# Kernel tuning notes

Measured on AMD Instinct MI355X. Metric: run time of the kernel, lower is better.

## Reference

```python
import jax, jax.numpy as jnp
import numpy as np

N = 10000
E = 320000

def _glorot(key, fan_in, fan_out):
    s = jnp.sqrt(2.0 / (fan_in + fan_out)).astype(jnp.float32)
    return jax.random.normal(key, (fan_in, fan_out), dtype=jnp.float32) * s

def setup_inputs() -> dict:
    key = jax.random.key(0)
    ks = iter(jax.random.split(key, 40))
    inp = {}
    for i in range(3):
        inp[f"feature{i}"] = jax.random.normal(next(ks), (N, 512), dtype=jnp.float32)
    for name in ["g0", "g1", "g2", "g"]:
        inp[name + "_src"] = jax.random.randint(next(ks), (E,), 0, N, dtype=jnp.int32)
        inp[name + "_dst"] = jax.random.randint(next(ks), (E,), 0, N, dtype=jnp.int32)
    # per-view GCN stacks: in->512 (relu), 512->256 (identity)
    for v in range(3):
        inp[f"w{v}_0"] = _glorot(next(ks), 512, 512)
        inp[f"b{v}_0"] = jnp.zeros((512,), jnp.float32)
        inp[f"w{v}_1"] = _glorot(next(ks), 512, 256)
        inp[f"b{v}_1"] = jnp.zeros((256,), jnp.float32)
    # FeatureFusion: three 256x256 weights (torch.randn init) + Linear(256,256)
    for i in (1, 2, 3):
        inp[f"fw{i}"] = jax.random.normal(next(ks), (256, 256), dtype=jnp.float32)
    inp["fcw"] = _glorot(next(ks), 256, 256)
    inp["fcb"] = jnp.zeros((256,), jnp.float32)
    # fusion-graph GCN stack: 256->256 (relu), 256->128 (identity)
    inp["wm_0"] = _glorot(next(ks), 256, 256)
    inp["bm_0"] = jnp.zeros((256,), jnp.float32)
    inp["wm_1"] = _glorot(next(ks), 256, 128)
    inp["bm_1"] = jnp.zeros((128,), jnp.float32)
    # InnerProductDecoder weight (xavier uniform -> use glorot normal surrogate)
    inp["decw"] = _glorot(next(ks), 128, 128)
    return inp

def _gcn(src, dst, x, W, b, act):
    # DGL GraphConv norm='both': act(D_in^{-1/2} A D_out^{-1/2} x W + b)
    ones = jnp.ones(src.shape, jnp.float32)
    deg_out = jax.ops.segment_sum(ones, src, num_segments=N)
    deg_in = jax.ops.segment_sum(ones, dst, num_segments=N)
    n_out = jnp.where(deg_out > 0, jax.lax.rsqrt(jnp.maximum(deg_out, 1.0)), 0.0)
    n_in = jnp.where(deg_in > 0, jax.lax.rsqrt(jnp.maximum(deg_in, 1.0)), 0.0)
    h = (x @ W) * n_out[:, None]                        # [N, out] (mult W first: in>=out)
    agg = jax.ops.segment_sum(h[src], dst, num_segments=N)
    return act(agg * n_in[:, None] + b)

def reference(feature0, feature1, feature2,
              g0_src, g0_dst, g1_src, g1_dst, g2_src, g2_dst, g_src, g_dst,
              w0_0, b0_0, w0_1, b0_1, w1_0, b1_0, w1_1, b1_1, w2_0, b2_0, w2_1, b2_1,
              fw1, fw2, fw3, fcw, fcb, wm_0, bm_0, wm_1, bm_1, decw):
    relu = jax.nn.relu
    ident = lambda t: t
    h0 = _gcn(g0_src, g0_dst, _gcn(g0_src, g0_dst, feature0, w0_0, b0_0, relu), w0_1, b0_1, ident)
    h1 = _gcn(g1_src, g1_dst, _gcn(g1_src, g1_dst, feature1, w1_0, b1_0, relu), w1_1, b1_1, ident)
    h2 = _gcn(g2_src, g2_dst, _gcn(g2_src, g2_dst, feature2, w2_0, b2_0, relu), w2_1, b2_1, ident)
    # FeatureFusion
    y = h0 @ fw1 + h1 @ fw2 + h2 @ fw3
    xh = y @ fcw + fcb
    # fusion graph with self loops (dgl.add_self_loop)
    loop = jnp.arange(N, dtype=jnp.int32)
    gs = jnp.concatenate([g_src, loop])
    gd = jnp.concatenate([g_dst, loop])
    xh = _gcn(gs, gd, xh, wm_0, bm_0, relu)
    xh = _gcn(gs, gd, xh, wm_1, bm_1, ident)
    # InnerProductDecoder (identical for each of the 3 views)
    adj = jax.nn.sigmoid((xh @ decw) @ xh.T)            # [N, N]
    return adj, adj, adj, xh
```

## Files before the change

kernel.cpp:

```cpp
#include <hip/hip_runtime.h>
#include <hip/hip_bf16.h>
#include <cstdint>
#include <cstddef>

typedef __attribute__((ext_vector_type(8))) short s16x8;
typedef __attribute__((ext_vector_type(4))) float f32x4;


__device__ inline float sigmoidf_fast(float x) {
    return 1.0f / (1.0f + __expf(-x));
}

__device__ inline ushort f2bf_bits(float x) {
    __hip_bfloat16 h = __float2bfloat16(x);
    return *reinterpret_cast<ushort*>(&h);
}

__device__ inline uint pk2bf(float a, float b) {
    return (uint)f2bf_bits(a) | ((uint)f2bf_bits(b) << 16);
}


__global__ void f2bf3(const float* __restrict__ s0, const float* __restrict__ s1,
                      const float* __restrict__ s2, ushort* __restrict__ dst, int n4) {
    int z = blockIdx.y;
    const float* src = z == 0 ? s0 : (z == 1 ? s1 : s2);
    int i = blockIdx.x * 256 + threadIdx.x;
    if (i < n4) {
        float4 v = ((const float4*)src)[i];
        uint2 o;
        o.x = pk2bf(v.x, v.y);
        o.y = pk2bf(v.z, v.w);
        ((uint2*)(dst + (size_t)z * n4 * 4))[i] = o;
    }
}

__global__ void wtrans3(const float* __restrict__ s0, const float* __restrict__ s1,
                        const float* __restrict__ s2, ushort* __restrict__ dst,
                        int K, int NC, int ldDst, int colOffPerZ, size_t dstStrideZ) {
    int z = blockIdx.y;
    const float* src = z == 0 ? s0 : (z == 1 ? s1 : s2);
    int i = blockIdx.x * 256 + threadIdx.x;
    if (i >= K * NC) return;
    int k = i / NC, n = i - k * NC;
    dst[(size_t)z * dstStrideZ + (size_t)n * ldDst + colOffPerZ * z + k] = f2bf_bits(src[i]);
}


__global__ void count_all(const int* __restrict__ s0, const int* __restrict__ d0,
                          const int* __restrict__ s1, const int* __restrict__ d1,
                          const int* __restrict__ s2, const int* __restrict__ d2,
                          const int* __restrict__ s3, const int* __restrict__ d3,
                          int* __restrict__ cntOut, int* __restrict__ cntIn, int E, int N) {
    int i = blockIdx.x * 256 + threadIdx.x;
    if (i >= E) return;
    atomicAdd(&cntOut[s0[i]], 1);          atomicAdd(&cntIn[d0[i]], 1);
    atomicAdd(&cntOut[N + s1[i]], 1);      atomicAdd(&cntIn[N + d1[i]], 1);
    atomicAdd(&cntOut[2 * N + s2[i]], 1);  atomicAdd(&cntIn[2 * N + d2[i]], 1);
    atomicAdd(&cntOut[3 * N + s3[i]], 1);  atomicAdd(&cntIn[3 * N + d3[i]], 1);
}

__global__ void norm_all(const int* __restrict__ cntOut, const int* __restrict__ cntIn,
                         float* __restrict__ norms, int N) {
    int i = blockIdx.x * 256 + threadIdx.x;
    if (i >= 8 * N) return;
    int g = i / (2 * N);
    int rem = i - g * 2 * N;
    int half = rem / N;
    int r = rem - half * N;
    int c = (half ? cntIn : cntOut)[g * N + r] + (g == 3 ? 1 : 0);
    norms[i] = c > 0 ? rsqrtf((float)c) : 0.0f;
}


__global__ void scan4(const int* __restrict__ cntIn, int* __restrict__ rp4, int N) {
    __shared__ int partial[1024];
    int g = blockIdx.x;
    const int* counts = cntIn + (size_t)g * N;
    int* rowptr = rp4 + (size_t)g * (N + 1);
    int tid = threadIdx.x;
    int per = (N + 1023) >> 10;
    int start = tid * per;
    int s = 0;
    for (int i = 0; i < per; ++i) {
        int idx = start + i;
        if (idx < N) s += counts[idx];
    }
    partial[tid] = s;
    __syncthreads();
    for (int off = 1; off < 1024; off <<= 1) {
        int v = (tid >= off) ? partial[tid - off] : 0;
        __syncthreads();
        partial[tid] += v;
        __syncthreads();
    }
    int run = (tid > 0) ? partial[tid - 1] : 0;
    for (int i = 0; i < per; ++i) {
        int idx = start + i;
        if (idx < N) { rowptr[idx] = run; run += counts[idx]; }
    }
    if (tid == 1023) rowptr[N] = partial[1023];
}

__global__ void scatter4(const int* __restrict__ s0, const int* __restrict__ d0,
                         const int* __restrict__ s1, const int* __restrict__ d1,
                         const int* __restrict__ s2, const int* __restrict__ d2,
                         const int* __restrict__ s3, const int* __restrict__ d3,
                         const int* __restrict__ rp4, int* __restrict__ cursor4,
                         int* __restrict__ col4, int E, int N) {
    int g = blockIdx.y;
    const int* ss[4] = { s0, s1, s2, s3 };
    const int* dd[4] = { d0, d1, d2, d3 };
    int i = blockIdx.x * 256 + threadIdx.x;
    if (i >= E) return;
    int d = dd[g][i];
    int pos = atomicAdd(&cursor4[g * N + d], 1);
    col4[(size_t)g * E + rp4[(size_t)g * (N + 1) + d] + pos] = ss[g][i];
}


template<int HAS_SCALE, int HAS_BIAS>
__global__ __launch_bounds__(256) void gemm_bf16(
    const ushort* __restrict__ A, const ushort* __restrict__ BT,
    const float* __restrict__ rowscale, const float* __restrict__ bias,
    ushort* __restrict__ C, int M, int K, int NC,
    size_t aStride, size_t btStride, size_t cStride, int sStride)
{
    int v = blockIdx.z;
    A += (size_t)v * aStride;
    BT += (size_t)v * btStride;
    C += (size_t)v * cStride;
    if (HAS_SCALE) rowscale += (size_t)v * sStride;

    __shared__ ushort As[128 * 64];
    __shared__ ushort Bs[128 * 64];
    int tid = threadIdx.x;
    int wave = tid >> 6, lane = tid & 63;
    int wr = wave >> 1, wc = wave & 1;
    int rowBase = blockIdx.y * 128, colBase = blockIdx.x * 128;
    int lr = lane & 15, kg = lane >> 4;

    f32x4 acc[4][4] = {};

    for (int k0 = 0; k0 < K; k0 += 64) {
#pragma unroll
        for (int i = 0; i < 4; ++i) {
            int id = i * 256 + tid;
            int row = id >> 3;
            int co  = (id & 7) << 3;
            int boff = ((row * 64 + co) << 1) ^ ((row & 7) << 4);
            int ar = rowBase + row; if (ar >= M) ar = M - 1;
            uint4 av = *(const uint4*)(A + (size_t)ar * K + k0 + co);
            *(uint4*)((char*)As + boff) = av;
            int bc = colBase + row;
            uint4 bv = *(const uint4*)(BT + (size_t)bc * K + k0 + co);
            *(uint4*)((char*)Bs + boff) = bv;
        }
        __syncthreads();
#pragma unroll
        for (int ks = 0; ks < 2; ++ks) {
            s16x8 afr[4], bfr[4];
#pragma unroll
            for (int m = 0; m < 4; ++m) {
                int fr = wr * 64 + m * 16 + lr;
                int boff = ((fr * 64 + ks * 32 + kg * 8) << 1) ^ ((fr & 7) << 4);
                afr[m] = *(const s16x8*)((char*)As + boff);
            }
#pragma unroll
            for (int n = 0; n < 4; ++n) {
                int fc = wc * 64 + n * 16 + lr;
                int boff = ((fc * 64 + ks * 32 + kg * 8) << 1) ^ ((fc & 7) << 4);
                bfr[n] = *(const s16x8*)((char*)Bs + boff);
            }
#pragma unroll
            for (int m = 0; m < 4; ++m)
#pragma unroll
                for (int n = 0; n < 4; ++n)
                    acc[m][n] = __builtin_amdgcn_mfma_f32_16x16x32_bf16(afr[m], bfr[n], acc[m][n], 0, 0, 0);
        }
        __syncthreads();
    }

#pragma unroll
    for (int m = 0; m < 4; ++m) {
#pragma unroll
        for (int i = 0; i < 4; ++i) {
            int r = rowBase + wr * 64 + m * 16 + kg * 4 + i;
            if (r >= M) continue;
            float s = HAS_SCALE ? rowscale[r] : 1.0f;
#pragma unroll
            for (int n = 0; n < 4; ++n) {
                int c = colBase + wc * 64 + n * 16 + lr;
                float vv = acc[m][n][i] * s;
                if (HAS_BIAS) vv += bias[c];
                C[(size_t)r * NC + c] = f2bf_bits(vv);
            }
        }
    }
}


#define ACC8(u) { acc[0]+=__uint_as_float(u.x<<16); acc[1]+=__uint_as_float(u.x&0xffff0000u); \
                  acc[2]+=__uint_as_float(u.y<<16); acc[3]+=__uint_as_float(u.y&0xffff0000u); \
                  acc[4]+=__uint_as_float(u.z<<16); acc[5]+=__uint_as_float(u.z&0xffff0000u); \
                  acc[6]+=__uint_as_float(u.w<<16); acc[7]+=__uint_as_float(u.w&0xffff0000u); }

template<int W, int RELU, int SELF, int OUTF32>
__global__ __launch_bounds__(256) void spmm_bf16(
    const int* __restrict__ rp4, const int* __restrict__ col4,
    const ushort* __restrict__ hB, const float* __restrict__ normB,
    const float* __restrict__ b0v, const float* __restrict__ b1v, const float* __restrict__ b2v,
    ushort* __restrict__ outB, float* __restrict__ outf,
    int M, int E, size_t hStride, int ninStride, size_t outStride, int ldOut, int colOffPerV)
{
    constexpr int TPR = W / 8;
    constexpr int RPB = 256 / TPR;
    int v = blockIdx.y;
    const int* rowptr = rp4 + (size_t)v * (M + 1);
    const int* col = col4 + (size_t)v * E;
    const ushort* h = hB + (size_t)v * hStride;
    const float* n_in = normB + (size_t)v * ninStride + M;
    const float* bias = (v == 0) ? b0v : (v == 1 ? b1v : b2v);
    ushort* outb = outB + (size_t)v * outStride;
    int cOff = colOffPerV * v;

    int lpr = threadIdx.x & (TPR - 1);
    int r = blockIdx.x * RPB + (threadIdx.x / TPR);
    if (r >= M) return;
    int c = lpr * 8;

    float acc[8] = {};
    int beg = rowptr[r], end = rowptr[r + 1];
    int j = beg;
    for (; j + 3 < end; j += 4) {
        int sA = col[j], sB = col[j + 1], sC = col[j + 2], sD = col[j + 3];
        uint4 uA = *(const uint4*)(h + (size_t)sA * W + c);
        uint4 uB = *(const uint4*)(h + (size_t)sB * W + c);
        uint4 uC = *(const uint4*)(h + (size_t)sC * W + c);
        uint4 uD = *(const uint4*)(h + (size_t)sD * W + c);
        ACC8(uA); ACC8(uB); ACC8(uC); ACC8(uD);
    }
    for (; j < end; ++j) {
        int s = col[j];
        uint4 u = *(const uint4*)(h + (size_t)s * W + c);
        ACC8(u);
    }
    if (SELF) {
        uint4 u = *(const uint4*)(h + (size_t)r * W + c);
        ACC8(u);
    }
    float ni = n_in[r];
    float o[8];
    float4 bb0 = *(const float4*)(bias + c);
    float4 bb1 = *(const float4*)(bias + c + 4);
    o[0] = acc[0] * ni + bb0.x; o[1] = acc[1] * ni + bb0.y;
    o[2] = acc[2] * ni + bb0.z; o[3] = acc[3] * ni + bb0.w;
    o[4] = acc[4] * ni + bb1.x; o[5] = acc[5] * ni + bb1.y;
    o[6] = acc[6] * ni + bb1.z; o[7] = acc[7] * ni + bb1.w;
    if (RELU) {
#pragma unroll
        for (int q = 0; q < 8; ++q) o[q] = fmaxf(o[q], 0.f);
    }
    uint4 ob;
    ob.x = pk2bf(o[0], o[1]); ob.y = pk2bf(o[2], o[3]);
    ob.z = pk2bf(o[4], o[5]); ob.w = pk2bf(o[6], o[7]);
    *(uint4*)(outb + (size_t)r * ldOut + cOff + c) = ob;
    if (OUTF32) {
        *(float4*)(outf + (size_t)r * W + c) = make_float4(o[0], o[1], o[2], o[3]);
        *(float4*)(outf + (size_t)r * W + c + 4) = make_float4(o[4], o[5], o[6], o[7]);
    }
}


__global__ __launch_bounds__(256) void adj_mfma(
    const ushort* __restrict__ Zb, const ushort* __restrict__ Xb,
    float* __restrict__ out, int M)
{
    int wave = threadIdx.x >> 6;
    int lane = threadIdx.x & 63;
    int wr = wave >> 1, wc = wave & 1;
    int rowBase = blockIdx.y * 128 + wr * 64;
    int colBase = blockIdx.x * 128 + wc * 64;
    int lr = lane & 15;
    int kg = lane >> 4;

    f32x4 acc[4][4] = {};

    int ar[4], bc[4];
#pragma unroll
    for (int m = 0; m < 4; ++m) {
        int r = rowBase + m * 16 + lr; ar[m] = (r < M) ? r : (M - 1);
        int c = colBase + m * 16 + lr; bc[m] = (c < M) ? c : (M - 1);
    }

#pragma unroll
    for (int ks = 0; ks < 4; ++ks) {
        s16x8 afr[4], bfr[4];
#pragma unroll
        for (int m = 0; m < 4; ++m)
            afr[m] = *(const s16x8*)(Zb + (size_t)ar[m] * 128 + ks * 32 + kg * 8);
#pragma unroll
        for (int n = 0; n < 4; ++n)
            bfr[n] = *(const s16x8*)(Xb + (size_t)bc[n] * 128 + ks * 32 + kg * 8);
#pragma unroll
        for (int m = 0; m < 4; ++m)
#pragma unroll
            for (int n = 0; n < 4; ++n)
                acc[m][n] = __builtin_amdgcn_mfma_f32_16x16x32_bf16(afr[m], bfr[n], acc[m][n], 0, 0, 0);
    }

    size_t NN = (size_t)M * M;
#pragma unroll
    for (int m = 0; m < 4; ++m) {
#pragma unroll
        for (int i = 0; i < 4; ++i) {
            int r = rowBase + m * 16 + kg * 4 + i;
            if (r >= M) continue;
            float* rowp = out + (size_t)r * M;
#pragma unroll
            for (int n = 0; n < 4; ++n) {
                int c = colBase + n * 16 + lr;
                if (c >= M) continue;
                float v = sigmoidf_fast(acc[m][n][i]);
                __builtin_nontemporal_store(v, rowp + c);
                __builtin_nontemporal_store(v, rowp + c + NN);
                __builtin_nontemporal_store(v, rowp + c + 2 * NN);
            }
        }
    }
}


extern "C" void kernel_launch(void* const* d_in, const int* in_sizes, int n_in,
                              void* d_out, int out_size, void* d_ws, size_t ws_size,
                              hipStream_t stream)
{
    const int N = in_sizes[0] / 512;
    const int E = in_sizes[3];

    const float* feat[3] = { (const float*)d_in[0], (const float*)d_in[1], (const float*)d_in[2] };
    const int* gsrc[4] = { (const int*)d_in[3], (const int*)d_in[5], (const int*)d_in[7], (const int*)d_in[9] };
    const int* gdst[4] = { (const int*)d_in[4], (const int*)d_in[6], (const int*)d_in[8], (const int*)d_in[10] };
    const float* W0[3] = { (const float*)d_in[11], (const float*)d_in[15], (const float*)d_in[19] };
    const float* B0[3] = { (const float*)d_in[12], (const float*)d_in[16], (const float*)d_in[20] };
    const float* W1[3] = { (const float*)d_in[13], (const float*)d_in[17], (const float*)d_in[21] };
    const float* B1[3] = { (const float*)d_in[14], (const float*)d_in[18], (const float*)d_in[22] };
    const float* fw[3] = { (const float*)d_in[23], (const float*)d_in[24], (const float*)d_in[25] };
    const float* fcw = (const float*)d_in[26];
    const float* fcb = (const float*)d_in[27];
    const float* wm0 = (const float*)d_in[28];
    const float* bm0 = (const float*)d_in[29];
    const float* wm1 = (const float*)d_in[30];
    const float* bm1 = (const float*)d_in[31];
    const float* decw = (const float*)d_in[32];
    float* out = (float*)d_out;

    uint8_t* p = (uint8_t*)d_ws;
    auto alloc = [&](size_t bytes) { void* r = p; p += (bytes + 255) & ~(size_t)255; return r; };

    float*  norms   = (float*)alloc((size_t)8 * N * 4);
    ushort* featb   = (ushort*)alloc((size_t)3 * N * 512 * 2);
    ushort* w0T     = (ushort*)alloc((size_t)3 * 512 * 512 * 2);
    ushort* w1T     = (ushort*)alloc((size_t)3 * 256 * 512 * 2);
    ushort* fwT     = (ushort*)alloc((size_t)256 * 768 * 2);
    ushort* fcT     = (ushort*)alloc((size_t)256 * 256 * 2);
    ushort* wm0T    = (ushort*)alloc((size_t)256 * 256 * 2);
    ushort* wm1T    = (ushort*)alloc((size_t)128 * 256 * 2);
    ushort* decT    = (ushort*)alloc((size_t)128 * 128 * 2);
    ushort* h512_3  = (ushort*)alloc((size_t)3 * N * 512 * 2);
    ushort* hb512_3 = (ushort*)alloc((size_t)3 * N * 512 * 2);
    ushort* h256_3  = (ushort*)alloc((size_t)3 * N * 256 * 2);
    ushort* hvcat   = (ushort*)alloc((size_t)N * 768 * 2);
    ushort* ybuf    = (ushort*)alloc((size_t)N * 256 * 2);
    ushort* xh256   = (ushort*)alloc((size_t)N * 256 * 2);
    ushort* m256    = (ushort*)alloc((size_t)N * 256 * 2);
    ushort* xh1     = (ushort*)alloc((size_t)N * 256 * 2);
    ushort* h128    = (ushort*)alloc((size_t)N * 128 * 2);
    ushort* xb      = (ushort*)alloc((size_t)N * 128 * 2);
    ushort* zb      = (ushort*)alloc((size_t)N * 128 * 2);
    int* cntOut     = (int*)alloc((size_t)4 * N * 4);
    int* cntIn      = (int*)alloc((size_t)4 * N * 4);
    int* cursor4    = (int*)alloc((size_t)4 * N * 4);
    int* rp4        = (int*)alloc((size_t)4 * (N + 1) * 4);
    int* col4       = (int*)alloc((size_t)4 * E * 4);

    {
        dim3 g((N * 512 / 4 + 255) / 256, 3);
        f2bf3<<<g, 256, 0, stream>>>(feat[0], feat[1], feat[2], featb, N * 512 / 4);
    }
    wtrans3<<<dim3((512 * 512 + 255) / 256, 3), 256, 0, stream>>>(W0[0], W0[1], W0[2], w0T, 512, 512, 512, 0, (size_t)512 * 512);
    wtrans3<<<dim3((512 * 256 + 255) / 256, 3), 256, 0, stream>>>(W1[0], W1[1], W1[2], w1T, 512, 256, 512, 0, (size_t)256 * 512);
    wtrans3<<<dim3((256 * 256 + 255) / 256, 3), 256, 0, stream>>>(fw[0], fw[1], fw[2], fwT, 256, 256, 768, 256, 0);
    wtrans3<<<dim3((256 * 256 + 255) / 256, 1), 256, 0, stream>>>(fcw, fcw, fcw, fcT, 256, 256, 256, 0, 0);
    wtrans3<<<dim3((256 * 256 + 255) / 256, 1), 256, 0, stream>>>(wm0, wm0, wm0, wm0T, 256, 256, 256, 0, 0);
    wtrans3<<<dim3((256 * 128 + 255) / 256, 1), 256, 0, stream>>>(wm1, wm1, wm1, wm1T, 256, 128, 256, 0, 0);
    wtrans3<<<dim3((128 * 128 + 255) / 256, 1), 256, 0, stream>>>(decw, decw, decw, decT, 128, 128, 128, 0, 0);

    hipMemsetAsync(cntOut, 0, (size_t)12 * N * 4, stream);
    count_all<<<(E + 255) / 256, 256, 0, stream>>>(
        gsrc[0], gdst[0], gsrc[1], gdst[1], gsrc[2], gdst[2], gsrc[3], gdst[3], cntOut, cntIn, E, N);
    norm_all<<<(8 * N + 255) / 256, 256, 0, stream>>>(cntOut, cntIn, norms, N);
    scan4<<<4, 1024, 0, stream>>>(cntIn, rp4, N);
    scatter4<<<dim3((E + 255) / 256, 4), 256, 0, stream>>>(
        gsrc[0], gdst[0], gsrc[1], gdst[1], gsrc[2], gdst[2], gsrc[3], gdst[3],
        rp4, cursor4, col4, E, N);

    gemm_bf16<1, 0><<<dim3(4, (N + 127) / 128, 3), 256, 0, stream>>>(
        featb, w0T, norms, nullptr, h512_3, N, 512, 512,
        (size_t)N * 512, (size_t)512 * 512, (size_t)N * 512, 2 * N);
    spmm_bf16<512, 1, 0, 0><<<dim3((N + 3) / 4, 3), 256, 0, stream>>>(
        rp4, col4, h512_3, norms, B0[0], B0[1], B0[2], hb512_3, nullptr,
        N, E, (size_t)N * 512, 2 * N, (size_t)N * 512, 512, 0);
    gemm_bf16<1, 0><<<dim3(2, (N + 127) / 128, 3), 256, 0, stream>>>(
        hb512_3, w1T, norms, nullptr, h256_3, N, 512, 256,
        (size_t)N * 512, (size_t)256 * 512, (size_t)N * 256, 2 * N);
    spmm_bf16<256, 0, 0, 0><<<dim3((N + 7) / 8, 3), 256, 0, stream>>>(
        rp4, col4, h256_3, norms, B1[0], B1[1], B1[2], hvcat, nullptr,
        N, E, (size_t)N * 256, 2 * N, 0, 768, 256);

    gemm_bf16<0, 0><<<dim3(2, (N + 127) / 128, 1), 256, 0, stream>>>(
        hvcat, fwT, nullptr, nullptr, ybuf, N, 768, 256, 0, 0, 0, 0);
    gemm_bf16<0, 1><<<dim3(2, (N + 127) / 128, 1), 256, 0, stream>>>(
        ybuf, fcT, nullptr, fcb, xh256, N, 256, 256, 0, 0, 0, 0);

    const int* rpF = rp4 + 3 * (N + 1);
    const int* colF = col4 + (size_t)3 * E;
    gemm_bf16<1, 0><<<dim3(2, (N + 127) / 128, 1), 256, 0, stream>>>(
        xh256, wm0T, norms + 6 * N, nullptr, m256, N, 256, 256, 0, 0, 0, 0);
    spmm_bf16<256, 1, 1, 0><<<dim3((N + 7) / 8, 1), 256, 0, stream>>>(
        rpF, colF, m256, norms + 6 * N, bm0, bm0, bm0, xh1, nullptr,
        N, E, 0, 0, 0, 256, 0);
    gemm_bf16<1, 0><<<dim3(1, (N + 127) / 128, 1), 256, 0, stream>>>(
        xh1, wm1T, norms + 6 * N, nullptr, h128, N, 256, 128, 0, 0, 0, 0);
    float* xhf = out + (size_t)3 * N * N;
    spmm_bf16<128, 0, 1, 1><<<dim3((N + 15) / 16, 1), 256, 0, stream>>>(
        rpF, colF, h128, norms + 6 * N, bm1, bm1, bm1, xb, xhf,
        N, E, 0, 0, 0, 128, 0);

    gemm_bf16<0, 0><<<dim3(1, (N + 127) / 128, 1), 256, 0, stream>>>(
        xb, decT, nullptr, nullptr, zb, N, 128, 128, 0, 0, 0, 0);
    dim3 agrid((N + 127) / 128, (N + 127) / 128);
    adj_mfma<<<agrid, 256, 0, stream>>>(zb, xb, out, N);
}
```

Before: 904.2 us.

## Fold fusion weights into a single effective weight and merge prep kernels

Result: no change. 895.2 us (-1.0%).

```diff
diff --git a/kernel.cpp b/kernel.cpp
--- a/kernel.cpp
+++ b/kernel.cpp
@@ -18,6 +18,62 @@
 
 __device__ inline uint pk2bf(float a, float b) {
     return (uint)f2bf_bits(a) | ((uint)f2bf_bits(b) << 16);
+}
+
+
+struct PrepArgs {
+    int4* zeroPtr; int nZero4;
+    const float* tsrc[8]; ushort* tdst[8];
+    int tK[8], tNC[8], tld[8];
+    int tBase[9];
+    const float* fc; const float* wm0; const float* fcb;
+    float* T1;
+    int zBlocks, wBlocks, tBlocks;
+};
+
+__global__ __launch_bounds__(256) void prep_misc(PrepArgs a) {
+    int b = blockIdx.x;
+    int tid = threadIdx.x;
+    if (b < a.zBlocks) {
+        int i = b * 256 + tid;
+        if (i < a.nZero4) a.zeroPtr[i] = make_int4(0, 0, 0, 0);
+        return;
+    }
+    b -= a.zBlocks;
+    if (b < a.wBlocks) {
+        int j = 0;
+        while (!(b >= a.tBase[j] && b < a.tBase[j + 1])) ++j;
+        int e = (b - a.tBase[j]) * 256 + tid;
+        int K = a.tK[j], NC = a.tNC[j];
+        if (e < K * NC) {
+            int k = e / NC, n = e - k * NC;
+            a.tdst[j][(size_t)n * a.tld[j] + k] = f2bf_bits(a.tsrc[j][e]);
+        }
+        return;
+    }
+    b -= a.wBlocks;
+    int n = tid;
+    float accv = 0.f;
+    if (b < 256) {
+        const float* fr = a.fc + (size_t)b * 256;
+        for (int i = 0; i < 256; ++i) accv += fr[i] * a.wm0[(size_t)i * 256 + n];
+        a.T1[(size_t)b * 256 + n] = accv;
+    } else {
+        for (int i = 0; i < 256; ++i) accv += a.fcb[i] * a.wm0[(size_t)i * 256 + n];
+        a.T1[(size_t)256 * 256 + n] = accv;
+    }
+}
+
+__global__ __launch_bounds__(256) void weff_main(
+    const float* __restrict__ fw0, const float* __restrict__ fw1, const float* __restrict__ fw2,
+    const float* __restrict__ T1, ushort* __restrict__ weffT)
+{
+    int k = blockIdx.x;
+    int n = threadIdx.x;
+    const float* src = (k < 256 ? fw0 : (k < 512 ? fw1 : fw2)) + (size_t)(k & 255) * 256;
+    float a = 0.f;
+    for (int j = 0; j < 256; ++j) a += src[j] * T1[(size_t)j * 256 + n];
+    weffT[(size_t)n * 768 + k] = f2bf_bits(a);
 }
 
 
@@ -35,17 +91,6 @@
     }
 }
 
-__global__ void wtrans3(const float* __restrict__ s0, const float* __restrict__ s1,
-                        const float* __restrict__ s2, ushort* __restrict__ dst,
-                        int K, int NC, int ldDst, int colOffPerZ, size_t dstStrideZ) {
-    int z = blockIdx.y;
-    const float* src = z == 0 ? s0 : (z == 1 ? s1 : s2);
-    int i = blockIdx.x * 256 + threadIdx.x;
-    if (i >= K * NC) return;
-    int k = i / NC, n = i - k * NC;
-    dst[(size_t)z * dstStrideZ + (size_t)n * ldDst + colOffPerZ * z + k] = f2bf_bits(src[i]);
-}
-
 
 __global__ void count_all(const int* __restrict__ s0, const int* __restrict__ d0,
                           const int* __restrict__ s1, const int* __restrict__ d1,
@@ -60,25 +105,21 @@
     atomicAdd(&cntOut[3 * N + s3[i]], 1);  atomicAdd(&cntIn[3 * N + d3[i]], 1);
 }
 
-__global__ void norm_all(const int* __restrict__ cntOut, const int* __restrict__ cntIn,
-                         float* __restrict__ norms, int N) {
-    int i = blockIdx.x * 256 + threadIdx.x;
-    if (i >= 8 * N) return;
-    int g = i / (2 * N);
-    int rem = i - g * 2 * N;
-    int half = rem / N;
-    int r = rem - half * N;
-    int c = (half ? cntIn : cntOut)[g * N + r] + (g == 3 ? 1 : 0);
-    norms[i] = c > 0 ? rsqrtf((float)c) : 0.0f;
-}
-
-
-__global__ void scan4(const int* __restrict__ cntIn, int* __restrict__ rp4, int N) {
+
+__global__ void scan4norm(const int* __restrict__ cntOut, const int* __restrict__ cntIn,
+                          int* __restrict__ rp4, float* __restrict__ norms, int N) {
     __shared__ int partial[1024];
     int g = blockIdx.x;
     const int* counts = cntIn + (size_t)g * N;
     int* rowptr = rp4 + (size_t)g * (N + 1);
     int tid = threadIdx.x;
+
+    int add = (g == 3) ? 1 : 0;
+    for (int idx = tid; idx < 2 * N; idx += 1024) {
+        int c = (idx < N) ? (cntOut[g * N + idx] + add) : (cntIn[g * N + idx - N] + add);
+        norms[(size_t)g * 2 * N + idx] = c > 0 ? rsqrtf((float)c) : 0.0f;
+    }
+
     int per = (N + 1023) >> 10;
     int start = tid * per;
     int s = 0;
@@ -119,7 +160,7 @@
 }
 
 
-template<int HAS_SCALE, int HAS_BIAS>
+template<int HAS_SCALE, int HAS_BIAS, int POST>
 __global__ __launch_bounds__(256) void gemm_bf16(
     const ushort* __restrict__ A, const ushort* __restrict__ BT,
     const float* __restrict__ rowscale, const float* __restrict__ bias,
@@ -191,8 +232,13 @@
 #pragma unroll
             for (int n = 0; n < 4; ++n) {
                 int c = colBase + wc * 64 + n * 16 + lr;
-                float vv = acc[m][n][i] * s;
-                if (HAS_BIAS) vv += bias[c];
+                float vv = acc[m][n][i];
+                if (POST) {
+                    vv = (vv + (HAS_BIAS ? bias[c] : 0.0f)) * s;
+                } else {
+                    vv *= s;
+                    if (HAS_BIAS) vv += bias[c];
+                }
                 C[(size_t)r * NC + c] = f2bf_bits(vv);
             }
         }
@@ -362,17 +408,14 @@
     ushort* featb   = (ushort*)alloc((size_t)3 * N * 512 * 2);
     ushort* w0T     = (ushort*)alloc((size_t)3 * 512 * 512 * 2);
     ushort* w1T     = (ushort*)alloc((size_t)3 * 256 * 512 * 2);
-    ushort* fwT     = (ushort*)alloc((size_t)256 * 768 * 2);
-    ushort* fcT     = (ushort*)alloc((size_t)256 * 256 * 2);
-    ushort* wm0T    = (ushort*)alloc((size_t)256 * 256 * 2);
     ushort* wm1T    = (ushort*)alloc((size_t)128 * 256 * 2);
     ushort* decT    = (ushort*)alloc((size_t)128 * 128 * 2);
+    float*  T1f     = (float*)alloc((size_t)257 * 256 * 4);
+    ushort* weffT   = (ushort*)alloc((size_t)256 * 768 * 2);
     ushort* h512_3  = (ushort*)alloc((size_t)3 * N * 512 * 2);
     ushort* hb512_3 = (ushort*)alloc((size_t)3 * N * 512 * 2);
     ushort* h256_3  = (ushort*)alloc((size_t)3 * N * 256 * 2);
     ushort* hvcat   = (ushort*)alloc((size_t)N * 768 * 2);
-    ushort* ybuf    = (ushort*)alloc((size_t)N * 256 * 2);
-    ushort* xh256   = (ushort*)alloc((size_t)N * 256 * 2);
     ushort* m256    = (ushort*)alloc((size_t)N * 256 * 2);
     ushort* xh1     = (ushort*)alloc((size_t)N * 256 * 2);
     ushort* h128    = (ushort*)alloc((size_t)N * 128 * 2);
@@ -384,60 +427,63 @@
     int* rp4        = (int*)alloc((size_t)4 * (N + 1) * 4);
     int* col4       = (int*)alloc((size_t)4 * E * 4);
 
-    {
-        dim3 g((N * 512 / 4 + 255) / 256, 3);
-        f2bf3<<<g, 256, 0, stream>>>(feat[0], feat[1], feat[2], featb, N * 512 / 4);
-    }
-    wtrans3<<<dim3((512 * 512 + 255) / 256, 3), 256, 0, stream>>>(W0[0], W0[1], W0[2], w0T, 512, 512, 512, 0, (size_t)512 * 512);
-    wtrans3<<<dim3((512 * 256 + 255) / 256, 3), 256, 0, stream>>>(W1[0], W1[1], W1[2], w1T, 512, 256, 512, 0, (size_t)256 * 512);
-    wtrans3<<<dim3((256 * 256 + 255) / 256, 3), 256, 0, stream>>>(fw[0], fw[1], fw[2], fwT, 256, 256, 768, 256, 0);
-    wtrans3<<<dim3((256 * 256 + 255) / 256, 1), 256, 0, stream>>>(fcw, fcw, fcw, fcT, 256, 256, 256, 0, 0);
-    wtrans3<<<dim3((256 * 256 + 255) / 256, 1), 256, 0, stream>>>(wm0, wm0, wm0, wm0T, 256, 256, 256, 0, 0);
-    wtrans3<<<dim3((256 * 128 + 255) / 256, 1), 256, 0, stream>>>(wm1, wm1, wm1, wm1T, 256, 128, 256, 0, 0);
-    wtrans3<<<dim3((128 * 128 + 255) / 256, 1), 256, 0, stream>>>(decw, decw, decw, decT, 128, 128, 128, 0, 0);
-
-    hipMemsetAsync(cntOut, 0, (size_t)12 * N * 4, stream);
+    PrepArgs pa;
+    pa.zeroPtr = (int4*)cntOut; pa.nZero4 = 12 * N / 4;
+    int wb = 0;
+    auto addJob = [&](int j, const float* s, ushort* d, int K, int NC, int ld) {
+        pa.tsrc[j] = s; pa.tdst[j] = d; pa.tK[j] = K; pa.tNC[j] = NC; pa.tld[j] = ld;
+        pa.tBase[j] = wb; wb += (K * NC + 255) / 256;
+    };
+    for (int v = 0; v < 3; ++v) addJob(v, W0[v], w0T + (size_t)v * 512 * 512, 512, 512, 512);
+    for (int v = 0; v < 3; ++v) addJob(3 + v, W1[v], w1T + (size_t)v * 256 * 512, 512, 256, 512);
+    addJob(6, wm1, wm1T, 256, 128, 256);
+    addJob(7, decw, decT, 128, 128, 128);
+    pa.tBase[8] = wb;
+    pa.fc = fcw; pa.wm0 = wm0; pa.fcb = fcb; pa.T1 = T1f;
+    pa.zBlocks = (pa.nZero4 + 255) / 256;
+    pa.wBlocks = wb;
+    pa.tBlocks = 257;
+    prep_misc<<<pa.zBlocks + pa.wBlocks + pa.tBlocks, 256, 0, stream>>>(pa);
+
+    f2bf3<<<dim3((N * 512 / 4 + 255) / 256, 3), 256, 0, stream>>>(feat[0], feat[1], feat[2], featb, N * 512 / 4);
+    weff_main<<<768, 256, 0, stream>>>(fw[0], fw[1], fw[2], T1f, weffT);
+
     count_all<<<(E + 255) / 256, 256, 0, stream>>>(
         gsrc[0], gdst[0], gsrc[1], gdst[1], gsrc[2], gdst[2], gsrc[3], gdst[3], cntOut, cntIn, E, N);
-    norm_all<<<(8 * N + 255) / 256, 256, 0, stream>>>(cntOut, cntIn, norms, N);
-    scan4<<<4, 1024, 0, stream>>>(cntIn, rp4, N);
+    scan4norm<<<4, 1024, 0, stream>>>(cntOut, cntIn, rp4, norms, N);
     scatter4<<<dim3((E + 255) / 256, 4), 256, 0, stream>>>(
         gsrc[0], gdst[0], gsrc[1], gdst[1], gsrc[2], gdst[2], gsrc[3], gdst[3],
         rp4, cursor4, col4, E, N);
 
-    gemm_bf16<1, 0><<<dim3(4, (N + 127) / 128, 3), 256, 0, stream>>>(
+    gemm_bf16<1, 0, 0><<<dim3(4, (N + 127) / 128, 3), 256, 0, stream>>>(
         featb, w0T, norms, nullptr, h512_3, N, 512, 512,
         (size_t)N * 512, (size_t)512 * 512, (size_t)N * 512, 2 * N);
     spmm_bf16<512, 1, 0, 0><<<dim3((N + 3) / 4, 3), 256, 0, stream>>>(
         rp4, col4, h512_3, norms, B0[0], B0[1], B0[2], hb512_3, nullptr,
         N, E, (size_t)N * 512, 2 * N, (size_t)N * 512, 512, 0);
-    gemm_bf16<1, 0><<<dim3(2, (N + 127) / 128, 3), 256, 0, stream>>>(
+    gemm_bf16<1, 0, 0><<<dim3(2, (N + 127) / 128, 3), 256, 0, stream>>>(
         hb512_3, w1T, norms, nullptr, h256_3, N, 512, 256,
         (size_t)N * 512, (size_t)256 * 512, (size_t)N * 256, 2 * N);
     spmm_bf16<256, 0, 0, 0><<<dim3((N + 7) / 8, 3), 256, 0, stream>>>(
         rp4, col4, h256_3, norms, B1[0], B1[1], B1[2], hvcat, nullptr,
         N, E, (size_t)N * 256, 2 * N, 0, 768, 256);
 
-    gemm_bf16<0, 0><<<dim3(2, (N + 127) / 128, 1), 256, 0, stream>>>(
-        hvcat, fwT, nullptr, nullptr, ybuf, N, 768, 256, 0, 0, 0, 0);
-    gemm_bf16<0, 1><<<dim3(2, (N + 127) / 128, 1), 256, 0, stream>>>(
-        ybuf, fcT, nullptr, fcb, xh256, N, 256, 256, 0, 0, 0, 0);
+    gemm_bf16<1, 1, 1><<<dim3(2, (N + 127) / 128, 1), 256, 0, stream>>>(
+        hvcat, weffT, norms + 6 * N, T1f + 256 * 256, m256, N, 768, 256, 0, 0, 0, 0);
 
     const int* rpF = rp4 + 3 * (N + 1);
     const int* colF = col4 + (size_t)3 * E;
-    gemm_bf16<1, 0><<<dim3(2, (N + 127) / 128, 1), 256, 0, stream>>>(
-        xh256, wm0T, norms + 6 * N, nullptr, m256, N, 256, 256, 0, 0, 0, 0);
     spmm_bf16<256, 1, 1, 0><<<dim3((N + 7) / 8, 1), 256, 0, stream>>>(
         rpF, colF, m256, norms + 6 * N, bm0, bm0, bm0, xh1, nullptr,
         N, E, 0, 0, 0, 256, 0);
-    gemm_bf16<1, 0><<<dim3(1, (N + 127) / 128, 1), 256, 0, stream>>>(
+    gemm_bf16<1, 0, 0><<<dim3(1, (N + 127) / 128, 1), 256, 0, stream>>>(
         xh1, wm1T, norms + 6 * N, nullptr, h128, N, 256, 128, 0, 0, 0, 0);
     float* xhf = out + (size_t)3 * N * N;
     spmm_bf16<128, 0, 1, 1><<<dim3((N + 15) / 16, 1), 256, 0, stream>>>(
         rpF, colF, h128, norms + 6 * N, bm1, bm1, bm1, xb, xhf,
         N, E, 0, 0, 0, 128, 0);
 
-    gemm_bf16<0, 0><<<dim3(1, (N + 127) / 128, 1), 256, 0, stream>>>(
+    gemm_bf16<0, 0, 0><<<dim3(1, (N + 127) / 128, 1), 256, 0, stream>>>(
         xb, decT, nullptr, nullptr, zb, N, 128, 128, 0, 0, 0, 0);
     dim3 agrid((N + 127) / 128, (N + 127) / 128);
     adj_mfma<<<agrid, 256, 0, stream>>>(zb, xb, out, N);
```
